# Performance work log

Measured on AMD Instinct MI355X. Metric: run time of the kernel, lower is better.

Reference implementation:

```python
import jax, jax.numpy as jnp
import numpy as np


def _binarize_topk_rows(probs, kn):
    # Row-wise top-k -> 1.0, else 0.0 (Binarize.forward, dim=1, int nei_k)
    e_n = probs.shape[0]
    _, idx = jax.lax.top_k(probs, kn)                      # [e_n, kn]
    binarized = jnp.zeros_like(probs)
    binarized = binarized.at[jnp.arange(e_n)[:, None], idx].set(1.0)
    return binarized


def _generate_G_from_H(H):
    # G = DV^-1/2 H W DE^-1 H^T DV^-1/2 with W = I, expressed as
    # elementwise row/col scaling around a single matmul (same math as the
    # original diag-matrix chain of 5 mm's).
    DV = jnp.sum(H, axis=1)                                # [v_n]  (W = ones)
    DE = jnp.sum(H, axis=0)                                # [e_n]
    invDE = jnp.where(DE > 0, 1.0 / DE, 0.0)               # isinf -> 0
    invDV = jnp.where(DV > 0, DV ** -0.5, 0.0)             # isinf -> 0
    Hs = (invDV[:, None] * H) * invDE[None, :]             # DV2 @ H @ W @ invDE
    G = (Hs @ H.T) * invDV[None, :]                        # ... @ H^T @ DV2
    return G


def setup_inputs() -> dict:
    key = jax.random.key(0)
    k1, k2 = jax.random.split(key)
    e_n, v_n = 4096, 16384
    vertex_assignment_map = jax.random.normal(k1, (e_n, v_n), dtype=jnp.float32)
    G = jax.random.normal(k2, (v_n, v_n), dtype=jnp.float32)
    return {"vertex_assignment_map": vertex_assignment_map, "G": G, "kn": 10}


def reference(vertex_assignment_map, G, kn):
    theta = 0.5
    # double softmax over the vertex dim, as in the original forward
    probs = jax.nn.softmax(vertex_assignment_map, axis=1)
    probs = jax.nn.softmax(probs, axis=-1)
    binarized = _binarize_topk_rows(probs, kn)             # [e_n, v_n]
    H = binarized.T                                        # [v_n, e_n]
    G_new = _generate_G_from_H(H)                          # [v_n, v_n]
    return (1.0 - theta) * G + theta * G_new
```

## Files before the change

### kernel.cpp

```cpp
#include <hip/hip_runtime.h>
#include <math.h>

#define VN 16384
#define EN 4096
#define TPB 256
#define CHUNKS 16

__global__ __launch_bounds__(TPB) void topk_dv_kernel(
    const float* __restrict__ vam, const int* __restrict__ kn_ptr,
    int* __restrict__ dv, int* __restrict__ topk)
{
    const int e = blockIdx.x;
    const int t = threadIdx.x;
    const float* row = vam + (size_t)e * VN;

    float v[CHUNKS][4];
#pragma unroll
    for (int c = 0; c < CHUNKS; ++c) {
        const float4 f = *reinterpret_cast<const float4*>(row + c * (TPB * 4) + t * 4);
        v[c][0] = f.x; v[c][1] = f.y; v[c][2] = f.z; v[c][3] = f.w;
    }

    int kn = kn_ptr[0];
    if (kn > 32) kn = 32;

    __shared__ unsigned long long wred[TPB / 64];
    __shared__ int bcast;

    for (int r = 0; r < kn; ++r) {
        float bv = -INFINITY;
        int   bi = 0;
#pragma unroll
        for (int c = 0; c < CHUNKS; ++c) {
#pragma unroll
            for (int j = 0; j < 4; ++j) {
                const int gi = c * (TPB * 4) + t * 4 + j;
                if (v[c][j] > bv) { bv = v[c][j]; bi = gi; }
            }
        }
        unsigned int uv = __float_as_uint(bv);
        uv = (uv & 0x80000000u) ? ~uv : (uv | 0x80000000u);
        unsigned long long key =
            ((unsigned long long)uv << 32) | (unsigned int)(~(unsigned int)bi);

#pragma unroll
        for (int s = 1; s < 64; s <<= 1) {
            const unsigned long long o = __shfl_xor(key, s, 64);
            if (o > key) key = o;
        }
        if ((t & 63) == 0) wred[t >> 6] = key;
        __syncthreads();
        if (t == 0) {
            unsigned long long kmax = wred[0];
#pragma unroll
            for (int w = 1; w < TPB / 64; ++w) if (wred[w] > kmax) kmax = wred[w];
            const int wi = (int)(~(unsigned int)(kmax & 0xffffffffull));
            bcast = wi;
            topk[(size_t)e * kn + r] = wi;
            atomicAdd(dv + wi, 1);
        }
        __syncthreads();
        const int wi = bcast;
#pragma unroll
        for (int c = 0; c < CHUNKS; ++c) {
#pragma unroll
            for (int j = 0; j < 4; ++j) {
                const int gi = c * (TPB * 4) + t * 4 + j;
                if (gi == wi) v[c][j] = -INFINITY;
            }
        }
        __syncthreads();
    }
}

__global__ void invdv_kernel(const int* __restrict__ dv, float* __restrict__ invdv)
{
    const int v = blockIdx.x * blockDim.x + threadIdx.x;
    if (v < VN) {
        const int d = dv[v];
        invdv[v] = d > 0 ? 1.0f / sqrtf((float)d) : 0.0f;
    }
}

__global__ void blend_kernel(const float4* __restrict__ g, float4* __restrict__ out)
{
    const long long n4 = (long long)VN * VN / 4;
    long long i = (long long)blockIdx.x * blockDim.x + threadIdx.x;
    const long long stride = (long long)gridDim.x * blockDim.x;
    for (; i < n4; i += stride) {
        float4 x = g[i];
        x.x *= 0.5f; x.y *= 0.5f; x.z *= 0.5f; x.w *= 0.5f;
        out[i] = x;
    }
}

__global__ void scatter_kernel(const int* __restrict__ topk,
                               const float* __restrict__ invdv,
                               const int* __restrict__ kn_ptr,
                               float* __restrict__ out)
{
    const int e = blockIdx.x;
    int kn = kn_ptr[0];
    if (kn > 32) kn = 32;
    const int total = kn * kn;
    const float inv_de = 1.0f / (float)kn;
    for (int p = threadIdx.x; p < total; p += blockDim.x) {
        const int a = topk[(size_t)e * kn + p / kn];
        const int b = topk[(size_t)e * kn + p % kn];
        const float c = 0.5f * invdv[a] * invdv[b] * inv_de;
        atomicAdd(out + (size_t)a * VN + b, c);
    }
}

extern "C" void kernel_launch(void* const* d_in, const int* in_sizes, int n_in,
                              void* d_out, int out_size, void* d_ws, size_t ws_size,
                              hipStream_t stream)
{
    const float* vam = (const float*)d_in[0];
    const float* G   = (const float*)d_in[1];
    const int*   kn  = (const int*)d_in[2];
    float* out = (float*)d_out;

    int*   dv    = (int*)d_ws;
    float* invdv = (float*)((char*)d_ws + (size_t)VN * 4);
    int*   topk  = (int*)((char*)d_ws + (size_t)VN * 8);

    hipMemsetAsync(dv, 0, VN * sizeof(int), stream);
    topk_dv_kernel<<<EN, TPB, 0, stream>>>(vam, kn, dv, topk);
    invdv_kernel<<<VN / 256, 256, 0, stream>>>(dv, invdv);
    blend_kernel<<<2048, 256, 0, stream>>>((const float4*)G, (float4*)out);
    scatter_kernel<<<EN, 128, 0, stream>>>(topk, invdv, kn, out);
}
```

Before: 603.4 us.

## Fuse blend into top-k kernel and rescan only the winning thread

The G*0.5 blend now runs inside the top-k kernel as extra blocks, interleaved 2:1 with top-k blocks, so the memory-bound copy overlaps the compute- and sync-heavy top-k selection. This removes a separate launch and the serialization between the two phases. The per-round local argmax is also cached, so after each round only the thread that owned the removed element rescans its 64 values. The interleaved grid makes all blocks compete for the same CUs, and the single-thread rescan adds a divergent serial step to each round.

```diff
diff --git a/kernel.cpp b/kernel.cpp
--- a/kernel.cpp
+++ b/kernel.cpp
@@ -5,13 +5,31 @@
 #define EN 4096
 #define TPB 256
 #define CHUNKS 16
+#define NBLEND 8192
+#define NBLOCKS (EN + NBLEND)
 
-__global__ __launch_bounds__(TPB) void topk_dv_kernel(
-    const float* __restrict__ vam, const int* __restrict__ kn_ptr,
-    int* __restrict__ dv, int* __restrict__ topk)
+__global__ __launch_bounds__(TPB) void fused_kernel(
+    const float* __restrict__ vam, const float4* __restrict__ g,
+    const int* __restrict__ kn_ptr,
+    int* __restrict__ dv, int* __restrict__ topk, float4* __restrict__ out)
 {
-    const int e = blockIdx.x;
+    const int bid = blockIdx.x;
     const int t = threadIdx.x;
+
+    if (bid % 3 != 0) {
+        const int blendId = 2 * (bid / 3) + (bid % 3 - 1);
+        const long long n4 = (long long)VN * VN / 4;
+        long long i = (long long)blendId * TPB + t;
+        const long long stride = (long long)NBLEND * TPB;
+        for (; i < n4; i += stride) {
+            float4 x = g[i];
+            x.x *= 0.5f; x.y *= 0.5f; x.z *= 0.5f; x.w *= 0.5f;
+            out[i] = x;
+        }
+        return;
+    }
+
+    const int e = bid / 3;
     const float* row = vam + (size_t)e * VN;
 
     float v[CHUNKS][4];
@@ -27,17 +45,18 @@
     __shared__ unsigned long long wred[TPB / 64];
     __shared__ int bcast;
 
+    float bv = -INFINITY;
+    int   bi = 0;
+#pragma unroll
+    for (int c = 0; c < CHUNKS; ++c) {
+#pragma unroll
+        for (int j = 0; j < 4; ++j) {
+            const int gi = c * (TPB * 4) + t * 4 + j;
+            if (v[c][j] > bv) { bv = v[c][j]; bi = gi; }
+        }
+    }
+
     for (int r = 0; r < kn; ++r) {
-        float bv = -INFINITY;
-        int   bi = 0;
-#pragma unroll
-        for (int c = 0; c < CHUNKS; ++c) {
-#pragma unroll
-            for (int j = 0; j < 4; ++j) {
-                const int gi = c * (TPB * 4) + t * 4 + j;
-                if (v[c][j] > bv) { bv = v[c][j]; bi = gi; }
-            }
-        }
         unsigned int uv = __float_as_uint(bv);
         uv = (uv & 0x80000000u) ? ~uv : (uv | 0x80000000u);
         unsigned long long key =
@@ -61,12 +80,24 @@
         }
         __syncthreads();
         const int wi = bcast;
+
+        if (((wi >> 2) & (TPB - 1)) == t) {
 #pragma unroll
-        for (int c = 0; c < CHUNKS; ++c) {
+            for (int c = 0; c < CHUNKS; ++c) {
 #pragma unroll
-            for (int j = 0; j < 4; ++j) {
-                const int gi = c * (TPB * 4) + t * 4 + j;
-                if (gi == wi) v[c][j] = -INFINITY;
+                for (int j = 0; j < 4; ++j) {
+                    const int gi = c * (TPB * 4) + t * 4 + j;
+                    if (gi == wi) v[c][j] = -INFINITY;
+                }
+            }
+            bv = -INFINITY; bi = 0;
+#pragma unroll
+            for (int c = 0; c < CHUNKS; ++c) {
+#pragma unroll
+                for (int j = 0; j < 4; ++j) {
+                    const int gi = c * (TPB * 4) + t * 4 + j;
+                    if (v[c][j] > bv) { bv = v[c][j]; bi = gi; }
+                }
             }
         }
         __syncthreads();
@@ -79,18 +110,6 @@
     if (v < VN) {
         const int d = dv[v];
         invdv[v] = d > 0 ? 1.0f / sqrtf((float)d) : 0.0f;
-    }
-}
-
-__global__ void blend_kernel(const float4* __restrict__ g, float4* __restrict__ out)
-{
-    const long long n4 = (long long)VN * VN / 4;
-    long long i = (long long)blockIdx.x * blockDim.x + threadIdx.x;
-    const long long stride = (long long)gridDim.x * blockDim.x;
-    for (; i < n4; i += stride) {
-        float4 x = g[i];
-        x.x *= 0.5f; x.y *= 0.5f; x.z *= 0.5f; x.w *= 0.5f;
-        out[i] = x;
     }
 }
 
@@ -126,8 +145,8 @@
     int*   topk  = (int*)((char*)d_ws + (size_t)VN * 8);
 
     hipMemsetAsync(dv, 0, VN * sizeof(int), stream);
-    topk_dv_kernel<<<EN, TPB, 0, stream>>>(vam, kn, dv, topk);
+    fused_kernel<<<NBLOCKS, TPB, 0, stream>>>(vam, (const float4*)G, kn, dv, topk,
+                                              (float4*)out);
     invdv_kernel<<<VN / 256, 256, 0, stream>>>(dv, invdv);
-    blend_kernel<<<2048, 256, 0, stream>>>((const float4*)G, (float4*)out);
     scatter_kernel<<<EN, 128, 0, stream>>>(topk, invdv, kn, out);
 }
```

New measurement: 524.5 us. 13.1% less time.
